# Kernel optimization log

Hardware: AMD Instinct MI355X
Metric: run time of the kernel (lower is better)

## Reference

```python
import jax, jax.numpy as jnp
import numpy as np
from jax import lax


def _conv(x, w, b):
    # 3x3 conv, stride 1, padding 1 == SAME; NCHW / OIHW layout like torch
    y = lax.conv_general_dilated(x, w, window_strides=(1, 1), padding='SAME',
                                 dimension_numbers=('NCHW', 'OIHW', 'NCHW'))
    return y + b[None, :, None, None]


def _maxpool2(x):
    return lax.reduce_window(x, -jnp.inf, lax.max, (1, 1, 2, 2), (1, 1, 2, 2), 'VALID')


def _upsample2(x):
    # nearest-neighbor upsample, scale factor 2
    return jnp.repeat(jnp.repeat(x, 2, axis=2), 2, axis=3)


def setup_inputs() -> dict:
    key = jax.random.key(0)
    ks = jax.random.split(key, 10)
    B, H, W = 128, 128, 128
    n_codes, d = 512, 32
    s = 0.1
    return {
        'x': jax.random.normal(ks[0], (B, 1, H, W), jnp.float32),
        'w1': jax.random.normal(ks[1], (16, 1, 3, 3), jnp.float32) * s,
        'b1': jnp.zeros((16,), jnp.float32),
        'w2': jax.random.normal(ks[2], (32, 16, 3, 3), jnp.float32) * s,
        'b2': jnp.zeros((32,), jnp.float32),
        'codebook': jax.random.normal(ks[3], (n_codes, d), jnp.float32),
        'w3': jax.random.normal(ks[4], (16, 32, 3, 3), jnp.float32) * s,
        'b3': jnp.zeros((16,), jnp.float32),
        'w4': jax.random.normal(ks[5], (1, 16, 3, 3), jnp.float32) * s,
        'b4': jnp.zeros((1,), jnp.float32),
    }


def reference(x, w1, b1, w2, b2, codebook, w3, b3, w4, b4):
    # encoder
    h = jax.nn.gelu(_maxpool2(_conv(x, w1, b1)), approximate=False)
    h = _maxpool2(_conv(h, w2, b2))  # [B, 32, H/4, W/4]
    B, C, Hq, Wq = h.shape

    # VectorQuantize: euclidean nearest-code lookup on flattened fmap
    z = h.transpose(0, 2, 3, 1).reshape(B, Hq * Wq, C)  # [B, N, d]
    d2 = ((z * z).sum(-1, keepdims=True)
          - 2.0 * jnp.einsum('bnc,kc->bnk', z, codebook)
          + (codebook * codebook).sum(-1))  # [B, N, K]
    idx = jnp.argmin(d2, axis=-1)  # [B, N]
    quant = codebook[idx]  # [B, N, d]
    commit_loss = jnp.mean((lax.stop_gradient(quant) - z) ** 2)
    indices = idx.reshape(B, Hq, Wq)

    # decoder: NOTE the source discards the quantized output (x_flat) and
    # keeps feeding the pre-quantization fmap h forward; we match that.
    g = jax.nn.gelu(_conv(_upsample2(h), w3, b3), approximate=False)
    out = jnp.clip(_conv(_upsample2(g), w4, b4), -1.0, 1.0)
    return out, indices, commit_loss
```

## Files before the change

### kernel.cpp

```cpp
#include <hip/hip_runtime.h>
#include <math.h>

typedef float f32x2 __attribute__((ext_vector_type(2)));

__device__ __forceinline__ float gelu_f(float x) {
    return 0.5f * x * (1.0f + erff(x * 0.7071067811865476f));
}

__global__ __launch_bounds__(256) void k_prep(const float* __restrict__ cb,
                                              const float* __restrict__ w3,
                                              const float* __restrict__ w4,
                                              float* __restrict__ ccp,
                                              float* __restrict__ w3t,
                                              float* __restrict__ w4t) {
    const int id = blockIdx.x * 256 + threadIdx.x;
    {
        const float* row = cb + id * 32;
        float s = 0.f;
#pragma unroll
        for (int c = 0; c < 32; ++c) s += row[c] * row[c];
        ccp[id] = s;
    }
    {
        const float* w = w3 + id * 9;
        const float T00 = w[0], T01 = w[1], T02 = w[2];
        const float T10 = w[3] + w[6], T11 = w[4] + w[7], T12 = w[5] + w[8];
        const float T20 = w[0] + w[3], T21 = w[1] + w[4], T22 = w[2] + w[5];
        const float T30 = w[6], T31 = w[7], T32 = w[8];
        float* o = w3t + id * 16;
        o[0] = T00; o[1] = T00 + T01; o[2] = T01 + T02; o[3] = T02;
        o[4] = T10; o[5] = T10 + T11; o[6] = T11 + T12; o[7] = T12;
        o[8] = T20; o[9] = T20 + T21; o[10] = T21 + T22; o[11] = T22;
        o[12] = T30; o[13] = T30 + T31; o[14] = T31 + T32; o[15] = T32;
    }
    if (id < 16) {
        const float* w = w4 + id * 9;
        const float T00 = w[0], T01 = w[1], T02 = w[2];
        const float T10 = w[3] + w[6], T11 = w[4] + w[7], T12 = w[5] + w[8];
        const float T20 = w[0] + w[3], T21 = w[1] + w[4], T22 = w[2] + w[5];
        const float T30 = w[6], T31 = w[7], T32 = w[8];
        float* o = w4t + id * 16;
        o[0] = T00; o[1] = T00 + T01; o[2] = T01 + T02; o[3] = T02;
        o[4] = T10; o[5] = T10 + T11; o[6] = T11 + T12; o[7] = T12;
        o[8] = T20; o[9] = T20 + T21; o[10] = T21 + T22; o[11] = T22;
        o[12] = T30; o[13] = T30 + T31; o[14] = T31 + T32; o[15] = T32;
    }
}

__global__ __launch_bounds__(256) void k_conv1(const float* __restrict__ x,
                                               const float* __restrict__ w1,
                                               const float* __restrict__ b1,
                                               float* __restrict__ h1) {
    __shared__ float xs[34 * 38];
    const int blk = blockIdx.x;
    const int b = blk >> 4;
    const int tile = blk & 15;
    const int ti = (tile >> 2) << 4, tj = (tile & 3) << 4;
    const int t = threadIdx.x;
    const float* xb = x + b * 16384;
    for (int i = t; i < 34 * 34; i += 256) {
        const int r = i / 34, c = i % 34;
        const int gr = 2 * ti - 1 + r, gc = 2 * tj - 1 + c;
        const float v = ((unsigned)gr < 128u && (unsigned)gc < 128u) ? xb[gr * 128 + gc] : 0.f;
        xs[r * 38 + (c & 1) * 19 + (c >> 1)] = v;
    }
    __syncthreads();
    const int jj = t & 15, ii = t >> 4;
    float pat[4][4];
#pragma unroll
    for (int r = 0; r < 4; r++) {
        const int row = (2 * ii + r) * 38;
        pat[r][0] = xs[row + jj];
        pat[r][1] = xs[row + 19 + jj];
        pat[r][2] = xs[row + jj + 1];
        pat[r][3] = xs[row + 20 + jj];
    }
    const int obase = b * 65536 + (ti + ii) * 64 + (tj + jj);
#pragma unroll 2
    for (int co = 0; co < 16; co++) {
        const float* wr = w1 + co * 9;
        float w[9];
#pragma unroll
        for (int k = 0; k < 9; k++) w[k] = wr[k];
        float s00 = 0.f, s01 = 0.f, s10 = 0.f, s11 = 0.f;
#pragma unroll
        for (int ty = 0; ty < 3; ty++)
#pragma unroll
            for (int tx = 0; tx < 3; tx++) {
                const float wv = w[ty * 3 + tx];
                s00 += wv * pat[ty][tx];
                s01 += wv * pat[ty][tx + 1];
                s10 += wv * pat[ty + 1][tx];
                s11 += wv * pat[ty + 1][tx + 1];
            }
        const float m = fmaxf(fmaxf(s00, s01), fmaxf(s10, s11)) + b1[co];
        h1[obase + co * 4096] = gelu_f(m);
    }
}

__global__ __launch_bounds__(256) void k_conv2(const float* __restrict__ h1,
                                               const float* __restrict__ w2,
                                               const float* __restrict__ b2,
                                               float* __restrict__ h) {
    __shared__ float hs[16 * 360];
    const int blk = blockIdx.x;
    const int b = blk >> 4;
    const int tile = blk & 15;
    const int ti = (tile >> 2) << 3, tj = (tile & 3) << 3;
    const int t = threadIdx.x;
    const float* h1b = h1 + b * 65536;
    for (int i = t; i < 16 * 324; i += 256) {
        const int ci = i / 324, rc = i % 324, r = rc / 18, c = rc % 18;
        const int gr = 2 * ti - 1 + r, gc = 2 * tj - 1 + c;
        const float v = ((unsigned)gr < 64u && (unsigned)gc < 64u) ? h1b[ci * 4096 + gr * 64 + gc] : 0.f;
        hs[ci * 360 + r * 20 + (c & 1) * 10 + (c >> 1)] = v;
    }
    __syncthreads();
    const int co0 = __builtin_amdgcn_readfirstlane((t >> 6) << 3);
    const int lane = t & 63;
    const int irow = lane >> 3, j = lane & 7;
    f32x2 A[8], B[8];
#pragma unroll
    for (int q = 0; q < 8; q++) { A[q] = (f32x2){0.f, 0.f}; B[q] = (f32x2){0.f, 0.f}; }
    const float* wbase = w2 + co0 * 144;
#pragma unroll 4
    for (int ci = 0; ci < 16; ci++) {
        f32x2 P[4][3];
#pragma unroll
        for (int r = 0; r < 4; r++) {
            const int row = ci * 360 + (2 * irow + r) * 20;
            const float e0 = hs[row + j];
            const float o0 = hs[row + 10 + j];
            const float e1 = hs[row + j + 1];
            const float o1 = hs[row + 11 + j];
            P[r][0] = (f32x2){e0, o0};
            P[r][1] = (f32x2){o0, e1};
            P[r][2] = (f32x2){e1, o1};
        }
#pragma unroll
        for (int q = 0; q < 8; q++) {
            const float* wr = wbase + q * 144 + ci * 9;
            float w[9];
#pragma unroll
            for (int k = 0; k < 9; k++) w[k] = wr[k];
#pragma unroll
            for (int ty = 0; ty < 3; ty++)
#pragma unroll
                for (int tx = 0; tx < 3; tx++) {
                    const float wv = w[ty * 3 + tx];
                    A[q] += P[ty][tx] * wv;
                    B[q] += P[ty + 1][tx] * wv;
                }
        }
    }
    float* hb = h + (b * 32 + co0) * 1024 + (ti + irow) * 32 + tj + j;
#pragma unroll
    for (int q = 0; q < 8; q++) {
        hb[q * 1024] = fmaxf(fmaxf(A[q].x, A[q].y), fmaxf(B[q].x, B[q].y)) + b2[co0 + q];
    }
}

__global__ __launch_bounds__(256) void k_vq_part(const float* __restrict__ h,
                                                 const float* __restrict__ cb,
                                                 const float* __restrict__ ccp,
                                                 float2* __restrict__ part) {
    const int blk = blockIdx.x;
    const int nchunk = blk >> 2, ks = blk & 3;
    const int t = threadIdx.x;
    const int n = nchunk * 256 + t;
    const int b = n >> 10, pos = n & 1023;
    const float* hb = h + b * 32768 + pos;
    float z[32];
    float zz = 0.f;
#pragma unroll
    for (int c = 0; c < 32; ++c) {
        z[c] = hb[c * 1024];
        zz += z[c] * z[c];
    }
    f32x2 z2[16];
#pragma unroll
    for (int i = 0; i < 16; ++i) z2[i] = (f32x2){z[2 * i], z[2 * i + 1]};
    const int kbase = ks << 7;
    const float* cbb = cb + (kbase << 5);
    const float* ccb = ccp + kbase;
    float bd = 3.4e38f;
    int bk = 0;
#pragma unroll 1
    for (int kk = 0; kk < 128; kk += 2) {
        const f32x2* r0 = (const f32x2*)(cbb + (kk << 5));
        const f32x2* r1 = (const f32x2*)(cbb + (kk << 5) + 32);
        f32x2 D0 = (f32x2){0.f, 0.f};
        f32x2 D1 = (f32x2){0.f, 0.f};
#pragma unroll
        for (int i = 0; i < 16; ++i) {
            D0 += z2[i] * r0[i];
            D1 += z2[i] * r1[i];
        }
        const float dot0 = D0.x + D0.y;
        const float dot1 = D1.x + D1.y;
        const float e0 = (zz - 2.f * dot0) + ccb[kk];
        const float e1 = (zz - 2.f * dot1) + ccb[kk + 1];
        if (e0 < bd) { bd = e0; bk = kbase + kk; }
        if (e1 < bd) { bd = e1; bk = kbase + kk + 1; }
    }
    part[ks * 131072 + n] = make_float2(bd, (float)bk);
}

__global__ __launch_bounds__(256) void k_vq_comb(const float2* __restrict__ part,
                                                 float* __restrict__ idx_out,
                                                 float* __restrict__ partials) {
    const int t = threadIdx.x;
    const int n = blockIdx.x * 256 + t;
    float2 p0 = part[n];
    float2 p1 = part[131072 + n];
    float2 p2 = part[262144 + n];
    float2 p3 = part[393216 + n];
    float bd = p0.x;
    float bk = p0.y;
    if (p1.x < bd) { bd = p1.x; bk = p1.y; }
    if (p2.x < bd) { bd = p2.x; bk = p2.y; }
    if (p3.x < bd) { bd = p3.x; bk = p3.y; }
    idx_out[n] = bk;
    __shared__ float red[256];
    red[t] = bd;
    __syncthreads();
    for (int off = 128; off > 0; off >>= 1) {
        if (t < off) red[t] += red[t + off];
        __syncthreads();
    }
    if (t == 0) partials[blockIdx.x] = red[0];
}

__global__ __launch_bounds__(256) void k_conv3(const float* __restrict__ h,
                                               const float* __restrict__ w3t,
                                               const float* __restrict__ b3,
                                               float* __restrict__ g) {
    __shared__ float hS[16 * 350];
    const int blk = blockIdx.x;
    const int b = blk >> 2, strip = blk & 3;
    const int i0 = strip * 8;
    const int t = threadIdx.x;
    const int co0 = __builtin_amdgcn_readfirstlane((t >> 6) << 2);
    const int lane = t & 63;
    const int rp = lane >> 3, cg = lane & 7;
    float acc[4][2][8];
#pragma unroll
    for (int cq = 0; cq < 4; cq++)
#pragma unroll
        for (int rr = 0; rr < 2; rr++)
#pragma unroll
            for (int u = 0; u < 8; u++) acc[cq][rr][u] = 0.f;
    const float* hb = h + b * 32768;
#pragma unroll 1
    for (int chunk = 0; chunk < 2; chunk++) {
        __syncthreads();
        for (int i = t; i < 16 * 340; i += 256) {
            const int cil = i / 340, rc = i % 340, r = rc / 34, c = rc % 34;
            const int gr = i0 - 1 + r, gc = c - 1;
            const float v = ((unsigned)gr < 32u && (unsigned)gc < 32u)
                ? hb[(chunk * 16 + cil) * 1024 + gr * 32 + gc] : 0.f;
            hS[cil * 350 + r * 35 + c] = v;
        }
        __syncthreads();
#pragma unroll 2
        for (int cil = 0; cil < 16; cil++) {
            const int ci = chunk * 16 + cil;
            float colr[3][6];
#pragma unroll
            for (int rr = 0; rr < 3; rr++) {
                const int rowb = cil * 350 + (rp + rr) * 35 + 4 * cg;
#pragma unroll
                for (int u = 0; u < 6; u++) colr[rr][u] = hS[rowb + u];
            }
#pragma unroll
            for (int cq = 0; cq < 4; cq++) {
                const float* wt = w3t + ((co0 + cq) * 32 + ci) * 16;
                const float T00 = wt[0], O00 = wt[1], E01 = wt[2], T02 = wt[3];
                const float T10 = wt[4], O10 = wt[5], E11 = wt[6], T12 = wt[7];
                const float T20 = wt[8], O20 = wt[9], E21 = wt[10], T22 = wt[11];
                const float T30 = wt[12], O30 = wt[13], E31 = wt[14], T32 = wt[15];
#pragma unroll
                for (int mm = 0; mm < 4; mm++) {
                    acc[cq][0][2 * mm]     += T00 * colr[0][mm] + E01 * colr[0][mm + 1] + T10 * colr[1][mm] + E11 * colr[1][mm + 1];
                    acc[cq][0][2 * mm + 1] += O00 * colr[0][mm + 1] + T02 * colr[0][mm + 2] + O10 * colr[1][mm + 1] + T12 * colr[1][mm + 2];
                    acc[cq][1][2 * mm]     += T20 * colr[1][mm] + E21 * colr[1][mm + 1] + T30 * colr[2][mm] + E31 * colr[2][mm + 1];
                    acc[cq][1][2 * mm + 1] += O20 * colr[1][mm + 1] + T22 * colr[1][mm + 2] + O30 * colr[2][mm + 1] + T32 * colr[2][mm + 2];
                }
            }
        }
    }
    const int p_e = strip * 16 + 2 * rp;
#pragma unroll
    for (int cq = 0; cq < 4; cq++) {
        const float bias = b3[co0 + cq];
        float* gb = g + (b * 16 + co0 + cq) * 4096 + p_e * 64 + 8 * cg;
#pragma unroll
        for (int rr = 0; rr < 2; rr++) {
            float4 v0, v1;
            v0.x = gelu_f(acc[cq][rr][0] + bias);
            v0.y = gelu_f(acc[cq][rr][1] + bias);
            v0.z = gelu_f(acc[cq][rr][2] + bias);
            v0.w = gelu_f(acc[cq][rr][3] + bias);
            v1.x = gelu_f(acc[cq][rr][4] + bias);
            v1.y = gelu_f(acc[cq][rr][5] + bias);
            v1.z = gelu_f(acc[cq][rr][6] + bias);
            v1.w = gelu_f(acc[cq][rr][7] + bias);
            *(float4*)(gb + rr * 64) = v0;
            *(float4*)(gb + rr * 64 + 4) = v1;
        }
    }
}

__global__ __launch_bounds__(256) void k_conv4(const float* __restrict__ g,
                                               const float* __restrict__ w4t,
                                               const float* __restrict__ b4,
                                               float* __restrict__ out) {
    __shared__ float gS[8 * 690];
    const int blk = blockIdx.x;
    const int b = blk >> 3, strip = blk & 7;
    const int i0 = strip * 8;
    const int t = threadIdx.x;
    const int rp = t >> 5, cg = t & 31;
    float acc[2][4];
#pragma unroll
    for (int rr = 0; rr < 2; rr++)
#pragma unroll
        for (int u = 0; u < 4; u++) acc[rr][u] = 0.f;
    const float* gbs = g + b * 65536;
#pragma unroll 1
    for (int chunk = 0; chunk < 2; chunk++) {
        __syncthreads();
        for (int i = t; i < 8 * 660; i += 256) {
            const int cil = i / 660, rc = i % 660, r = rc / 66, c = rc % 66;
            const int gr = i0 - 1 + r, gc = c - 1;
            const float v = ((unsigned)gr < 64u && (unsigned)gc < 64u)
                ? gbs[(chunk * 8 + cil) * 4096 + gr * 64 + gc] : 0.f;
            gS[cil * 690 + r * 69 + c] = v;
        }
        __syncthreads();
#pragma unroll 2
        for (int cil = 0; cil < 8; cil++) {
            const int ci = chunk * 8 + cil;
            float colv[3][4];
#pragma unroll
            for (int rr = 0; rr < 3; rr++) {
                const int rowb = cil * 690 + (rp + rr) * 69 + 2 * cg;
#pragma unroll
                for (int u = 0; u < 4; u++) colv[rr][u] = gS[rowb + u];
            }
            const float* wt = w4t + ci * 16;
            const float T00 = wt[0], O00 = wt[1], E01 = wt[2], T02 = wt[3];
            const float T10 = wt[4], O10 = wt[5], E11 = wt[6], T12 = wt[7];
            const float T20 = wt[8], O20 = wt[9], E21 = wt[10], T22 = wt[11];
            const float T30 = wt[12], O30 = wt[13], E31 = wt[14], T32 = wt[15];
#pragma unroll
            for (int mm = 0; mm < 2; mm++) {
                acc[0][2 * mm]     += T00 * colv[0][mm] + E01 * colv[0][mm + 1] + T10 * colv[1][mm] + E11 * colv[1][mm + 1];
                acc[0][2 * mm + 1] += O00 * colv[0][mm + 1] + T02 * colv[0][mm + 2] + O10 * colv[1][mm + 1] + T12 * colv[1][mm + 2];
                acc[1][2 * mm]     += T20 * colv[1][mm] + E21 * colv[1][mm + 1] + T30 * colv[2][mm] + E31 * colv[2][mm + 1];
                acc[1][2 * mm + 1] += O20 * colv[1][mm + 1] + T22 * colv[1][mm + 2] + O30 * colv[2][mm + 1] + T32 * colv[2][mm + 2];
            }
        }
    }
    const float bias = b4[0];
    const int p_e = strip * 16 + 2 * rp;
    float* ob = out + b * 16384 + p_e * 128 + 4 * cg;
#pragma unroll
    for (int rr = 0; rr < 2; rr++) {
        float4 v;
        v.x = fminf(fmaxf(acc[rr][0] + bias, -1.f), 1.f);
        v.y = fminf(fmaxf(acc[rr][1] + bias, -1.f), 1.f);
        v.z = fminf(fmaxf(acc[rr][2] + bias, -1.f), 1.f);
        v.w = fminf(fmaxf(acc[rr][3] + bias, -1.f), 1.f);
        *(float4*)(ob + rr * 128) = v;
    }
}

__global__ __launch_bounds__(256) void k_reduce(const float* __restrict__ partials,
                                                float* __restrict__ loss) {
    __shared__ float red[256];
    const int t = threadIdx.x;
    float s = 0.f;
    for (int i = t; i < 512; i += 256) s += partials[i];
    red[t] = s;
    __syncthreads();
    for (int off = 128; off > 0; off >>= 1) {
        if (t < off) red[t] += red[t + off];
        __syncthreads();
    }
    if (t == 0) loss[0] = red[0] * (1.0f / 4194304.0f);
}

extern "C" void kernel_launch(void* const* d_in, const int* in_sizes, int n_in,
                              void* d_out, int out_size, void* d_ws, size_t ws_size,
                              hipStream_t stream) {
    const float* x  = (const float*)d_in[0];
    const float* w1 = (const float*)d_in[1];
    const float* b1 = (const float*)d_in[2];
    const float* w2 = (const float*)d_in[3];
    const float* b2 = (const float*)d_in[4];
    const float* cb = (const float*)d_in[5];
    const float* w3 = (const float*)d_in[6];
    const float* b3 = (const float*)d_in[7];
    const float* w4 = (const float*)d_in[8];
    const float* b4 = (const float*)d_in[9];

    float* ws = (float*)d_ws;
    float* h1 = ws;
    float* h  = ws + 8388608;
    float* g  = h1;
    float2* part = (float2*)ws;
    float* ccp = ws + 12582912;
    float* pa  = ws + 12583424;
    float* w3t = ws + 12583936;
    float* w4t = ws + 12592128;
    float* outp = (float*)d_out;

    k_prep<<<2, 256, 0, stream>>>(cb, w3, w4, ccp, w3t, w4t);
    k_conv1<<<2048, 256, 0, stream>>>(x, w1, b1, h1);
    k_conv2<<<2048, 256, 0, stream>>>(h1, w2, b2, h);
    k_vq_part<<<2048, 256, 0, stream>>>(h, cb, ccp, part);
    k_vq_comb<<<512, 256, 0, stream>>>(part, outp + 2097152, pa);
    k_conv3<<<512, 256, 0, stream>>>(h, w3t, b3, g);
    k_conv4<<<1024, 256, 0, stream>>>(g, w4t, b4, outp);
    k_reduce<<<1, 256, 0, stream>>>(pa, outp + 2228224);
}
```

Before: 239.0 us.

## Merge stages into four kernels, fuse VQ combine, and pre-splat conv2 weights

Kernels go from eight launches to four by adding extra block ranges. Weight prep runs inside the conv1 launch, the VQ search shares a launch with conv3, and the loss reduction rides along with conv4. The VQ split over the codebook now happens across the four waves of one block, and the argmin combine is done in shared memory. That removes the partial-result buffer round trip and the separate combine kernel. Conv2 weights are pre-duplicated into float pairs so the packed FMA can take vector operands directly. Some scratch (w3t, w2d) is placed inside the output buffer before the final output overwrites it, which relies on that launch ordering.

```diff
diff --git a/kernel.cpp b/kernel.cpp
--- a/kernel.cpp
+++ b/kernel.cpp
@@ -7,56 +7,63 @@
     return 0.5f * x * (1.0f + erff(x * 0.7071067811865476f));
 }
 
-__global__ __launch_bounds__(256) void k_prep(const float* __restrict__ cb,
-                                              const float* __restrict__ w3,
-                                              const float* __restrict__ w4,
-                                              float* __restrict__ ccp,
-                                              float* __restrict__ w3t,
-                                              float* __restrict__ w4t) {
-    const int id = blockIdx.x * 256 + threadIdx.x;
-    {
-        const float* row = cb + id * 32;
-        float s = 0.f;
-#pragma unroll
-        for (int c = 0; c < 32; ++c) s += row[c] * row[c];
-        ccp[id] = s;
-    }
-    {
-        const float* w = w3 + id * 9;
-        const float T00 = w[0], T01 = w[1], T02 = w[2];
-        const float T10 = w[3] + w[6], T11 = w[4] + w[7], T12 = w[5] + w[8];
-        const float T20 = w[0] + w[3], T21 = w[1] + w[4], T22 = w[2] + w[5];
-        const float T30 = w[6], T31 = w[7], T32 = w[8];
-        float* o = w3t + id * 16;
-        o[0] = T00; o[1] = T00 + T01; o[2] = T01 + T02; o[3] = T02;
-        o[4] = T10; o[5] = T10 + T11; o[6] = T11 + T12; o[7] = T12;
-        o[8] = T20; o[9] = T20 + T21; o[10] = T21 + T22; o[11] = T22;
-        o[12] = T30; o[13] = T30 + T31; o[14] = T31 + T32; o[15] = T32;
-    }
-    if (id < 16) {
-        const float* w = w4 + id * 9;
-        const float T00 = w[0], T01 = w[1], T02 = w[2];
-        const float T10 = w[3] + w[6], T11 = w[4] + w[7], T12 = w[5] + w[8];
-        const float T20 = w[0] + w[3], T21 = w[1] + w[4], T22 = w[2] + w[5];
-        const float T30 = w[6], T31 = w[7], T32 = w[8];
-        float* o = w4t + id * 16;
-        o[0] = T00; o[1] = T00 + T01; o[2] = T01 + T02; o[3] = T02;
-        o[4] = T10; o[5] = T10 + T11; o[6] = T11 + T12; o[7] = T12;
-        o[8] = T20; o[9] = T20 + T21; o[10] = T21 + T22; o[11] = T22;
-        o[12] = T30; o[13] = T30 + T31; o[14] = T31 + T32; o[15] = T32;
-    }
-}
-
-__global__ __launch_bounds__(256) void k_conv1(const float* __restrict__ x,
-                                               const float* __restrict__ w1,
-                                               const float* __restrict__ b1,
-                                               float* __restrict__ h1) {
+__global__ __launch_bounds__(256) void kA(const float* __restrict__ x,
+                                          const float* __restrict__ w1,
+                                          const float* __restrict__ b1,
+                                          float* __restrict__ h1,
+                                          const float* __restrict__ cb,
+                                          const float* __restrict__ w3,
+                                          const float* __restrict__ w4,
+                                          float* __restrict__ ccp,
+                                          float* __restrict__ w3t,
+                                          float* __restrict__ w4t,
+                                          f32x2* __restrict__ w2d,
+                                          const float* __restrict__ w2) {
+    const int blk = blockIdx.x;
+    const int t = threadIdx.x;
+    if (blk >= 2048) {
+        const int id = (blk - 2048) * 256 + t;
+        {
+            const float* row = cb + id * 32;
+            float s = 0.f;
+#pragma unroll
+            for (int c = 0; c < 32; ++c) s += row[c] * row[c];
+            ccp[id] = s;
+        }
+        {
+            const float* w = w3 + id * 9;
+            const float T00 = w[0], T01 = w[1], T02 = w[2];
+            const float T10 = w[3] + w[6], T11 = w[4] + w[7], T12 = w[5] + w[8];
+            const float T20 = w[0] + w[3], T21 = w[1] + w[4], T22 = w[2] + w[5];
+            const float T30 = w[6], T31 = w[7], T32 = w[8];
+            float* o = w3t + id * 16;
+            o[0] = T00; o[1] = T00 + T01; o[2] = T01 + T02; o[3] = T02;
+            o[4] = T10; o[5] = T10 + T11; o[6] = T11 + T12; o[7] = T12;
+            o[8] = T20; o[9] = T20 + T21; o[10] = T21 + T22; o[11] = T22;
+            o[12] = T30; o[13] = T30 + T31; o[14] = T31 + T32; o[15] = T32;
+        }
+        if (id < 16) {
+            const float* w = w4 + id * 9;
+            const float T00 = w[0], T01 = w[1], T02 = w[2];
+            const float T10 = w[3] + w[6], T11 = w[4] + w[7], T12 = w[5] + w[8];
+            const float T20 = w[0] + w[3], T21 = w[1] + w[4], T22 = w[2] + w[5];
+            const float T30 = w[6], T31 = w[7], T32 = w[8];
+            float* o = w4t + id * 16;
+            o[0] = T00; o[1] = T00 + T01; o[2] = T01 + T02; o[3] = T02;
+            o[4] = T10; o[5] = T10 + T11; o[6] = T11 + T12; o[7] = T12;
+            o[8] = T20; o[9] = T20 + T21; o[10] = T21 + T22; o[11] = T22;
+            o[12] = T30; o[13] = T30 + T31; o[14] = T31 + T32; o[15] = T32;
+        }
+        for (int i = id; i < 4608; i += 512) {
+            const float wv = w2[i];
+            w2d[i] = (f32x2){wv, wv};
+        }
+        return;
+    }
     __shared__ float xs[34 * 38];
-    const int blk = blockIdx.x;
     const int b = blk >> 4;
     const int tile = blk & 15;
     const int ti = (tile >> 2) << 4, tj = (tile & 3) << 4;
-    const int t = threadIdx.x;
     const float* xb = x + b * 16384;
     for (int i = t; i < 34 * 34; i += 256) {
         const int r = i / 34, c = i % 34;
@@ -99,7 +106,7 @@
 }
 
 __global__ __launch_bounds__(256) void k_conv2(const float* __restrict__ h1,
-                                               const float* __restrict__ w2,
+                                               const f32x2* __restrict__ w2d,
                                                const float* __restrict__ b2,
                                                float* __restrict__ h) {
     __shared__ float hs[16 * 360];
@@ -122,7 +129,7 @@
     f32x2 A[8], B[8];
 #pragma unroll
     for (int q = 0; q < 8; q++) { A[q] = (f32x2){0.f, 0.f}; B[q] = (f32x2){0.f, 0.f}; }
-    const float* wbase = w2 + co0 * 144;
+    const f32x2* wbase = w2d + co0 * 144;
 #pragma unroll 4
     for (int ci = 0; ci < 16; ci++) {
         f32x2 P[4][3];
@@ -139,17 +146,16 @@
         }
 #pragma unroll
         for (int q = 0; q < 8; q++) {
-            const float* wr = wbase + q * 144 + ci * 9;
-            float w[9];
-#pragma unroll
-            for (int k = 0; k < 9; k++) w[k] = wr[k];
+            const f32x2* wr = wbase + q * 144 + ci * 9;
+            f32x2 W[9];
+#pragma unroll
+            for (int k = 0; k < 9; k++) W[k] = wr[k];
 #pragma unroll
             for (int ty = 0; ty < 3; ty++)
 #pragma unroll
                 for (int tx = 0; tx < 3; tx++) {
-                    const float wv = w[ty * 3 + tx];
-                    A[q] += P[ty][tx] * wv;
-                    B[q] += P[ty + 1][tx] * wv;
+                    A[q] += P[ty][tx] * W[ty * 3 + tx];
+                    B[q] += P[ty + 1][tx] * W[ty * 3 + tx];
                 }
         }
     }
@@ -160,86 +166,80 @@
     }
 }
 
-__global__ __launch_bounds__(256) void k_vq_part(const float* __restrict__ h,
-                                                 const float* __restrict__ cb,
-                                                 const float* __restrict__ ccp,
-                                                 float2* __restrict__ part) {
+__global__ __launch_bounds__(256) void kB(const float* __restrict__ h,
+                                          const float* __restrict__ w3t,
+                                          const float* __restrict__ b3,
+                                          float* __restrict__ g,
+                                          const float* __restrict__ cb,
+                                          const float* __restrict__ ccp,
+                                          float* __restrict__ idx_out,
+                                          float* __restrict__ pa) {
+    __shared__ float smem[16 * 350];
     const int blk = blockIdx.x;
-    const int nchunk = blk >> 2, ks = blk & 3;
     const int t = threadIdx.x;
-    const int n = nchunk * 256 + t;
-    const int b = n >> 10, pos = n & 1023;
-    const float* hb = h + b * 32768 + pos;
-    float z[32];
-    float zz = 0.f;
-#pragma unroll
-    for (int c = 0; c < 32; ++c) {
-        z[c] = hb[c * 1024];
-        zz += z[c] * z[c];
-    }
-    f32x2 z2[16];
-#pragma unroll
-    for (int i = 0; i < 16; ++i) z2[i] = (f32x2){z[2 * i], z[2 * i + 1]};
-    const int kbase = ks << 7;
-    const float* cbb = cb + (kbase << 5);
-    const float* ccb = ccp + kbase;
-    float bd = 3.4e38f;
-    int bk = 0;
+    if (blk >= 512) {
+        const int vblk = blk - 512;
+        const int n0 = vblk * 64;
+        const int wave = t >> 6, lane = t & 63;
+        const int n = n0 + lane;
+        const int b = n >> 10, pos = n & 1023;
+        const float* hb = h + b * 32768 + pos;
+        float z[32];
+        float zz = 0.f;
+#pragma unroll
+        for (int c = 0; c < 32; ++c) {
+            z[c] = hb[c * 1024];
+            zz += z[c] * z[c];
+        }
+        f32x2 z2[16];
+#pragma unroll
+        for (int i = 0; i < 16; ++i) z2[i] = (f32x2){z[2 * i], z[2 * i + 1]};
+        const int kbase = wave << 7;
+        const float* cbb = cb + (kbase << 5);
+        const float* ccb = ccp + kbase;
+        float bd = 3.4e38f;
+        int bk = 0;
 #pragma unroll 1
-    for (int kk = 0; kk < 128; kk += 2) {
-        const f32x2* r0 = (const f32x2*)(cbb + (kk << 5));
-        const f32x2* r1 = (const f32x2*)(cbb + (kk << 5) + 32);
-        f32x2 D0 = (f32x2){0.f, 0.f};
-        f32x2 D1 = (f32x2){0.f, 0.f};
-#pragma unroll
-        for (int i = 0; i < 16; ++i) {
-            D0 += z2[i] * r0[i];
-            D1 += z2[i] * r1[i];
-        }
-        const float dot0 = D0.x + D0.y;
-        const float dot1 = D1.x + D1.y;
-        const float e0 = (zz - 2.f * dot0) + ccb[kk];
-        const float e1 = (zz - 2.f * dot1) + ccb[kk + 1];
-        if (e0 < bd) { bd = e0; bk = kbase + kk; }
-        if (e1 < bd) { bd = e1; bk = kbase + kk + 1; }
-    }
-    part[ks * 131072 + n] = make_float2(bd, (float)bk);
-}
-
-__global__ __launch_bounds__(256) void k_vq_comb(const float2* __restrict__ part,
-                                                 float* __restrict__ idx_out,
-                                                 float* __restrict__ partials) {
-    const int t = threadIdx.x;
-    const int n = blockIdx.x * 256 + t;
-    float2 p0 = part[n];
-    float2 p1 = part[131072 + n];
-    float2 p2 = part[262144 + n];
-    float2 p3 = part[393216 + n];
-    float bd = p0.x;
-    float bk = p0.y;
-    if (p1.x < bd) { bd = p1.x; bk = p1.y; }
-    if (p2.x < bd) { bd = p2.x; bk = p2.y; }
-    if (p3.x < bd) { bd = p3.x; bk = p3.y; }
-    idx_out[n] = bk;
-    __shared__ float red[256];
-    red[t] = bd;
-    __syncthreads();
-    for (int off = 128; off > 0; off >>= 1) {
-        if (t < off) red[t] += red[t + off];
-        __syncthreads();
-    }
-    if (t == 0) partials[blockIdx.x] = red[0];
-}
-
-__global__ __launch_bounds__(256) void k_conv3(const float* __restrict__ h,
-                                               const float* __restrict__ w3t,
-                                               const float* __restrict__ b3,
-                                               float* __restrict__ g) {
-    __shared__ float hS[16 * 350];
-    const int blk = blockIdx.x;
+        for (int kk = 0; kk < 128; kk += 2) {
+            const f32x2* r0 = (const f32x2*)(cbb + (kk << 5));
+            const f32x2* r1 = (const f32x2*)(cbb + (kk << 5) + 32);
+            f32x2 D0 = (f32x2){0.f, 0.f};
+            f32x2 D1 = (f32x2){0.f, 0.f};
+#pragma unroll
+            for (int i = 0; i < 16; ++i) {
+                D0 += z2[i] * r0[i];
+                D1 += z2[i] * r1[i];
+            }
+            const float dot0 = D0.x + D0.y;
+            const float dot1 = D1.x + D1.y;
+            const float e0 = (zz - 2.f * dot0) + ccb[kk];
+            const float e1 = (zz - 2.f * dot1) + ccb[kk + 1];
+            if (e0 < bd) { bd = e0; bk = kbase + kk; }
+            if (e1 < bd) { bd = e1; bk = kbase + kk + 1; }
+        }
+        float2* sm = (float2*)smem;
+        sm[wave * 64 + lane] = make_float2(bd, (float)bk);
+        __syncthreads();
+        if (t < 64) {
+            float2 p0 = sm[t];
+            float2 p1 = sm[64 + t];
+            float2 p2 = sm[128 + t];
+            float2 p3 = sm[192 + t];
+            float fd = p0.x, fk = p0.y;
+            if (p1.x < fd) { fd = p1.x; fk = p1.y; }
+            if (p2.x < fd) { fd = p2.x; fk = p2.y; }
+            if (p3.x < fd) { fd = p3.x; fk = p3.y; }
+            idx_out[n0 + t] = fk;
+            float s = fd;
+#pragma unroll
+            for (int m = 1; m < 64; m <<= 1) s += __shfl_xor(s, m, 64);
+            if (t == 0) pa[vblk] = s;
+        }
+        return;
+    }
+    float* hS = smem;
     const int b = blk >> 2, strip = blk & 3;
     const int i0 = strip * 8;
-    const int t = threadIdx.x;
     const int co0 = __builtin_amdgcn_readfirstlane((t >> 6) << 2);
     const int lane = t & 63;
     const int rp = lane >> 3, cg = lane & 7;
@@ -311,15 +311,30 @@
     }
 }
 
-__global__ __launch_bounds__(256) void k_conv4(const float* __restrict__ g,
-                                               const float* __restrict__ w4t,
-                                               const float* __restrict__ b4,
-                                               float* __restrict__ out) {
-    __shared__ float gS[8 * 690];
+__global__ __launch_bounds__(256) void kC(const float* __restrict__ g,
+                                          const float* __restrict__ w4t,
+                                          const float* __restrict__ b4,
+                                          float* __restrict__ out,
+                                          const float* __restrict__ pa,
+                                          float* __restrict__ loss) {
+    __shared__ float smem[8 * 690];
     const int blk = blockIdx.x;
+    const int t = threadIdx.x;
+    if (blk >= 1024) {
+        float s = 0.f;
+        for (int i = t; i < 2048; i += 256) s += pa[i];
+        smem[t] = s;
+        __syncthreads();
+        for (int off = 128; off > 0; off >>= 1) {
+            if (t < off) smem[t] += smem[t + off];
+            __syncthreads();
+        }
+        if (t == 0) loss[0] = smem[0] * (1.0f / 4194304.0f);
+        return;
+    }
+    float* gS = smem;
     const int b = blk >> 3, strip = blk & 7;
     const int i0 = strip * 8;
-    const int t = threadIdx.x;
     const int rp = t >> 5, cg = t & 31;
     float acc[2][4];
 #pragma unroll
@@ -374,21 +389,6 @@
         v.w = fminf(fmaxf(acc[rr][3] + bias, -1.f), 1.f);
         *(float4*)(ob + rr * 128) = v;
     }
-}
-
-__global__ __launch_bounds__(256) void k_reduce(const float* __restrict__ partials,
-                                                float* __restrict__ loss) {
-    __shared__ float red[256];
-    const int t = threadIdx.x;
-    float s = 0.f;
-    for (int i = t; i < 512; i += 256) s += partials[i];
-    red[t] = s;
-    __syncthreads();
-    for (int off = 128; off > 0; off >>= 1) {
-        if (t < off) red[t] += red[t + off];
-        __syncthreads();
-    }
-    if (t == 0) loss[0] = red[0] * (1.0f / 4194304.0f);
 }
 
 extern "C" void kernel_launch(void* const* d_in, const int* in_sizes, int n_in,
@@ -409,19 +409,18 @@
     float* h1 = ws;
     float* h  = ws + 8388608;
     float* g  = h1;
-    float2* part = (float2*)ws;
     float* ccp = ws + 12582912;
     float* pa  = ws + 12583424;
-    float* w3t = ws + 12583936;
-    float* w4t = ws + 12592128;
+    float* w4t = ws + 12585472;
+
     float* outp = (float*)d_out;
-
-    k_prep<<<2, 256, 0, stream>>>(cb, w3, w4, ccp, w3t, w4t);
-    k_conv1<<<2048, 256, 0, stream>>>(x, w1, b1, h1);
-    k_conv2<<<2048, 256, 0, stream>>>(h1, w2, b2, h);
-    k_vq_part<<<2048, 256, 0, stream>>>(h, cb, ccp, part);
-    k_vq_comb<<<512, 256, 0, stream>>>(part, outp + 2097152, pa);
-    k_conv3<<<512, 256, 0, stream>>>(h, w3t, b3, g);
-    k_conv4<<<1024, 256, 0, stream>>>(g, w4t, b4, outp);
-    k_reduce<<<1, 256, 0, stream>>>(pa, outp + 2228224);
-}
+    float* w3t = outp;
+    f32x2* w2d = (f32x2*)(outp + 8192);
+    float* idx = outp + 2097152;
+    float* loss = outp + 2228224;
+
+    kA<<<2050, 256, 0, stream>>>(x, w1, b1, h1, cb, w3, w4, ccp, w3t, w4t, w2d, w2);
+    k_conv2<<<2048, 256, 0, stream>>>(h1, w2d, b2, h);
+    kB<<<2560, 256, 0, stream>>>(h, w3t, b3, g, cb, ccp, idx, pa);
+    kC<<<1025, 256, 0, stream>>>(g, w4t, b4, outp, pa, loss);
+}
```

New measurement: 359.9 us. 50.6% more time.
